# Performance work log

Hardware: AMD Instinct MI355X
Metric: run time of the kernel (lower is better)

Reference implementation:

```python
import jax, jax.numpy as jnp
import numpy as np

B, D, NH = 32768, 32, 128
SCALE = 0.05  # weight init scale; keeps exp(s) well-conditioned


def setup_inputs() -> dict:
    key = jax.random.key(0)
    ks = jax.random.split(key, 10)
    x = jax.random.normal(ks[0], (B, D), jnp.float32)
    # layer 0: LeafParam(2) -> learned constant (s, t)
    p0 = jax.random.normal(ks[1], (2,), jnp.float32) * SCALE
    # per-dim MLPs for i = 1..D-1, stacked. Layer i consumes x[:, :i]; we pad
    # its first weight to (D, NH) with rows >= i zeroed so a single batched
    # einsum computes all per-dim nets at once (same math as the python loop).
    mask = (jnp.arange(D)[None, :] < jnp.arange(1, D)[:, None]).astype(jnp.float32)  # (D-1, D)
    W1 = jax.random.normal(ks[2], (D - 1, D, NH), jnp.float32) * SCALE * mask[:, :, None]
    b1 = jax.random.normal(ks[3], (D - 1, NH), jnp.float32) * SCALE
    W2 = jax.random.normal(ks[4], (D - 1, NH, NH), jnp.float32) * SCALE
    b2 = jax.random.normal(ks[5], (D - 1, NH), jnp.float32) * SCALE
    W3 = jax.random.normal(ks[6], (D - 1, NH, NH), jnp.float32) * SCALE
    b3 = jax.random.normal(ks[7], (D - 1, NH), jnp.float32) * SCALE
    W4 = jax.random.normal(ks[8], (D - 1, NH, 2), jnp.float32) * SCALE
    b4 = jax.random.normal(ks[9], (D - 1, 2), jnp.float32) * SCALE
    return dict(x=x, p0=p0, W1=W1, b1=b1, W2=W2, b2=b2, W3=W3, b3=b3, W4=W4, b4=b4)


def _lrelu(h):
    return jnp.where(h >= 0, h, 0.2 * h)  # LeakyReLU(0.2)


def reference(x, p0, W1, b1, W2, b2, W3, b3, W4, b4):
    # All D-1 per-dim MLPs in parallel. W1 rows >= i are zero, so
    h = _lrelu(jnp.einsum('bd,idh->bih', x, W1) + b1[None])     # (B, D-1, NH)
    h = _lrelu(jnp.einsum('bih,ihk->bik', h, W2) + b2[None])
    h = _lrelu(jnp.einsum('bih,ihk->bik', h, W3) + b3[None])
    st = jnp.einsum('bih,iho->bio', h, W4) + b4[None]           # (B, D-1, 2)
    st0 = jnp.broadcast_to(p0[None, None, :], (x.shape[0], 1, 2))
    st = jnp.concatenate([st0, st], axis=1)                     # (B, D, 2)
    s, t = st[..., 0], st[..., 1]
    z = x * jnp.exp(s) + t      # parity=True -> order is the identity permutation
    log_det = jnp.sum(s, axis=1)                                # (B,)
    return z, log_det
```

## Files before the change

### kernel.cpp

```cpp
#include <hip/hip_runtime.h>

typedef __bf16 v8bf  __attribute__((ext_vector_type(8)));
typedef float  f32x4  __attribute__((ext_vector_type(4)));
typedef float  f32x16 __attribute__((ext_vector_type(16)));
typedef unsigned int u32;
typedef u32 u32x4 __attribute__((ext_vector_type(4)));
typedef unsigned short u16;

#define NI   31
#define DD   32
#define NHID 128
#define NROW 32768
#define NCHUNK 32
#define ITERS  4
#define NET_EL 36864
#define W2F_EL 4096
#define W3F_EL 20480
#define LDS_W4T 73728
#define LDS_BB  74240
#define LDS_BYTES 75008

__device__ __forceinline__ u32 cvtpk(float lo, float hi) {
    u32 r;
    asm("v_cvt_pk_bf16_f32 %0, %1, %2" : "=v"(r) : "v"(lo), "v"(hi));
    return r;
}

__device__ __forceinline__ void repack_tile(const f32x16 c, v8bf* f0, v8bf* f1) {
    f32x16 v;
    #pragma unroll
    for (int r = 0; r < 16; ++r) { float x = c[r]; v[r] = fmaxf(x, 0.2f * x); }
    #pragma unroll
    for (int p = 0; p < 2; ++p) {
        u32 a0 = cvtpk(v[8*p + 0], v[8*p + 1]);
        u32 a1 = cvtpk(v[8*p + 2], v[8*p + 3]);
        u32 b0 = cvtpk(v[8*p + 4], v[8*p + 5]);
        u32 b1 = cvtpk(v[8*p + 6], v[8*p + 7]);
        asm("v_permlane32_swap_b32 %0, %1" : "+v"(a0), "+v"(b0));
        asm("v_permlane32_swap_b32 %0, %1" : "+v"(a1), "+v"(b1));
        u32x4 wd = {a0, a1, b0, b1};
        if (p == 0) *f0 = __builtin_bit_cast(v8bf, wd);
        else        *f1 = __builtin_bit_cast(v8bf, wd);
    }
}

__global__ void maf_prep(const float* __restrict__ W1, const float* __restrict__ W2,
                         const float* __restrict__ W3, __bf16* __restrict__ blob,
                         __bf16* __restrict__ xfrag, float* __restrict__ xT,
                         const float* __restrict__ x, const float* __restrict__ p0,
                         float* __restrict__ zout, float* __restrict__ ldout) {
    int b = blockIdx.x, t = threadIdx.x;
    if (b < 3 * NI) {
        __shared__ float panel[16 * 128];
        int kind = b / NI, i = b % NI;
        const float* src; __bf16* dst; int NKS;
        if (kind == 0)      { src = W2 + (size_t)i * NHID * NHID; dst = blob + (size_t)i * NET_EL + W2F_EL; NKS = 8; }
        else if (kind == 1) { src = W3 + (size_t)i * NHID * NHID; dst = blob + (size_t)i * NET_EL + W3F_EL; NKS = 8; }
        else                { src = W1 + (size_t)i * DD * NHID;   dst = blob + (size_t)i * NET_EL;          NKS = 2; }
        const int fo = t & 127, hi2 = t >> 7;
        const int mt = fo >> 5, c = fo & 31;
        for (int ksb = 0; ksb < NKS; ++ksb) {
            #pragma unroll
            for (int r = 0; r < 8; ++r) {
                int e = r * 256 + t;
                panel[e] = src[(size_t)(ksb * 16 + (e >> 7)) * NHID + (e & 127)];
            }
            __syncthreads();
            __bf16 tmp[8];
            #pragma unroll
            for (int j = 0; j < 8; ++j) tmp[j] = (__bf16)panel[(hi2 * 8 + j) * 128 + fo];
            *(u32x4*)&dst[((size_t)(mt * NKS + ksb) * 64 + hi2 * 32 + c) * 8] = *(u32x4*)tmp;
            __syncthreads();
        }
    } else {
        __shared__ float pan[64 * 33];
        const int xb = b - 3 * NI;
        const float s0 = p0[0], t0 = p0[1];
        const float es = expf(s0);
        for (int pass = 0; pass < 4; ++pass) {
            const int rb = xb * 256 + pass * 64;
            #pragma unroll
            for (int r = 0; r < 8; ++r) {
                int e = r * 256 + t;
                pan[(e >> 5) * 33 + (e & 31)] = x[(size_t)(rb + (e >> 5)) * DD + (e & 31)];
            }
            __syncthreads();
            {
                int row = t & 63, dbase = (t >> 6) * 8;
                #pragma unroll
                for (int dd = 0; dd < 8; ++dd)
                    xT[(size_t)(dbase + dd) * NROW + rb + row] = pan[row * 33 + dbase + dd];
            }
            {
                int w2 = t >> 6, l = t & 63;
                int nt = w2 >> 1, ks = w2 & 1;
                int c = l & 31, hi = l >> 5;
                const float* pr = &pan[(nt * 32 + c) * 33 + ks * 16 + hi * 8];
                f32x4 x0 = *(const f32x4*)pr;
                f32x4 x1 = *(const f32x4*)(pr + 4);
                u32x4 wd = {cvtpk(x0[0], x0[1]), cvtpk(x0[2], x0[3]),
                            cvtpk(x1[0], x1[1]), cvtpk(x1[2], x1[3])};
                *(u32x4*)&xfrag[(size_t)(rb >> 6) * 2048 + ((w2 * 64 + l) << 3)] = wd;
            }
            if (t < 64) {
                int row = rb + t;
                ldout[row] = s0;
                zout[(size_t)row * DD] = pan[t * 33] * es + t0;
            }
            __syncthreads();
        }
    }
}

__global__ __launch_bounds__(256, 2) void maf_main(
    const __bf16* __restrict__ xfrag, const float* __restrict__ xT,
    const __bf16* __restrict__ blob,
    const float* __restrict__ b1, const float* __restrict__ b2,
    const float* __restrict__ b3,
    const float* __restrict__ W4, const float* __restrict__ b4,
    float* __restrict__ zout, float* __restrict__ ldout) {

    extern __shared__ __align__(16) char smem[];
    __bf16* w4t = (__bf16*)(smem + LDS_W4T);
    __bf16* bb  = (__bf16*)(smem + LDS_BB);
    const __bf16* wlds = (const __bf16*)smem;

    const int t = threadIdx.x;
    const int i = blockIdx.x / NCHUNK;
    const int chunk = blockIdx.x % NCHUNK;
    const int l = t & 63, w = t >> 6, c = l & 31, hi = l >> 5;
    const bool full_k1 = (i >= 16);

    {
        const u32x4* src = (const u32x4*)(blob + (size_t)i * NET_EL);
        u32x4* dst = (u32x4*)smem;
        #pragma unroll
        for (int k = 0; k < 18; ++k) dst[k * 256 + t] = src[k * 256 + t];
        w4t[t] = (__bf16)W4[(size_t)i * 2 * NHID + (t & 127) * 2 + (t >> 7)];
        if (t < NHID) {
            bb[t]       = (__bf16)b1[i * NHID + t];
            bb[128 + t] = (__bf16)b2[i * NHID + t];
            bb[256 + t] = (__bf16)b3[i * NHID + t];
        }
    }
    __syncthreads();

    const u32 ones0 = (hi == 0) ? 0x3F80u : 0u;
    const v8bf Bones = __builtin_bit_cast(v8bf, (u32x4){ones0, 0u, 0u, 0u});
    const float s0 = b4[2 * i], t0 = b4[2 * i + 1];
    const f32x16 zz = {};

    f32x16 acc[4][2];
    v8bf Bf[2][8];
    v8bf Bx[2][2];

#define LOADX(G)                                                                      \
    { const __bf16* xg = xfrag + (size_t)(G) * 2048;                                  \
      Bx[0][0] = *(const v8bf*)&xg[(0 * 64 + l) << 3];                                \
      if (full_k1) Bx[0][1] = *(const v8bf*)&xg[(1 * 64 + l) << 3];                   \
      Bx[1][0] = *(const v8bf*)&xg[(2 * 64 + l) << 3];                                \
      if (full_k1) Bx[1][1] = *(const v8bf*)&xg[(3 * 64 + l) << 3]; }

#define ABIAS(BOFF, MT)                                                               \
    __builtin_bit_cast(v8bf, (u32x4){                                                 \
        (hi == 0) ? (u32)__builtin_bit_cast(u16, bb[(BOFF) + (MT) * 32 + c]) : 0u,    \
        0u, 0u, 0u})

#define HIDDEN(BASE_EL, BOFF)                                                         \
    {                                                                                 \
        _Pragma("unroll")                                                             \
        for (int mt = 0; mt < 4; ++mt) {                                              \
            v8bf Ab = ABIAS(BOFF, mt);                                                \
            acc[mt][0] = __builtin_amdgcn_mfma_f32_32x32x16_bf16(Ab, Bones, zz, 0, 0, 0); \
            acc[mt][1] = __builtin_amdgcn_mfma_f32_32x32x16_bf16(Ab, Bones, zz, 0, 0, 0); \
        }                                                                             \
        _Pragma("unroll")                                                             \
        for (int ks = 0; ks < 8; ++ks) {                                              \
            v8bf A[4];                                                                \
            _Pragma("unroll")                                                         \
            for (int mt = 0; mt < 4; ++mt)                                            \
                A[mt] = *(const v8bf*)&wlds[(BASE_EL) + ((mt * 8 + ks) * 64 + l) * 8]; \
            _Pragma("unroll")                                                         \
            for (int mt = 0; mt < 4; ++mt)                                            \
                _Pragma("unroll")                                                     \
                for (int nt = 0; nt < 2; ++nt)                                        \
                    acc[mt][nt] = __builtin_amdgcn_mfma_f32_32x32x16_bf16(            \
                        A[mt], Bf[nt][ks], acc[mt][nt], 0, 0, 0);                     \
        }                                                                             \
        _Pragma("unroll")                                                             \
        for (int mt = 0; mt < 4; ++mt)                                                \
            _Pragma("unroll")                                                         \
            for (int nt = 0; nt < 2; ++nt)                                            \
                repack_tile(acc[mt][nt], &Bf[nt][2 * mt], &Bf[nt][2 * mt + 1]);       \
    }

    LOADX((chunk * 1024 + w * 64) >> 6)

    for (int it = 0; it < ITERS; ++it) {
        const int row0 = chunk * 1024 + it * 256 + w * 64;

        #pragma unroll
        for (int mt = 0; mt < 4; ++mt) {
            v8bf Ab = ABIAS(0, mt);
            v8bf A0 = *(const v8bf*)&wlds[((mt * 2 + 0) * 64 + l) * 8];
            v8bf A1;
            if (full_k1) A1 = *(const v8bf*)&wlds[((mt * 2 + 1) * 64 + l) * 8];
            #pragma unroll
            for (int nt = 0; nt < 2; ++nt) {
                f32x16 a = __builtin_amdgcn_mfma_f32_32x32x16_bf16(Ab, Bones, zz, 0, 0, 0);
                a = __builtin_amdgcn_mfma_f32_32x32x16_bf16(A0, Bx[nt][0], a, 0, 0, 0);
                if (full_k1)
                    a = __builtin_amdgcn_mfma_f32_32x32x16_bf16(A1, Bx[nt][1], a, 0, 0, 0);
                acc[mt][nt] = a;
            }
        }
        #pragma unroll
        for (int mt = 0; mt < 4; ++mt)
            #pragma unroll
            for (int nt = 0; nt < 2; ++nt)
                repack_tile(acc[mt][nt], &Bf[nt][2 * mt], &Bf[nt][2 * mt + 1]);

        if (it + 1 < ITERS)
            LOADX((chunk * 1024 + (it + 1) * 256 + w * 64) >> 6)

        HIDDEN(W2F_EL, 128)
        HIDDEN(W3F_EL, 256)

        {
            f32x16 acc4[2];
            acc4[0] = zz; acc4[1] = zz;
            #pragma unroll
            for (int ks = 0; ks < 8; ++ks) {
                v8bf a4 = {};
                if (c < 2) a4 = *(const v8bf*)&w4t[c * NHID + ks * 16 + hi * 8];
                acc4[0] = __builtin_amdgcn_mfma_f32_32x32x16_bf16(a4, Bf[0][ks], acc4[0], 0, 0, 0);
                acc4[1] = __builtin_amdgcn_mfma_f32_32x32x16_bf16(a4, Bf[1][ks], acc4[1], 0, 0, 0);
            }
            if (hi == 0) {
                #pragma unroll
                for (int nt = 0; nt < 2; ++nt) {
                    int row = row0 + nt * 32 + c;
                    float s  = acc4[nt][0] + s0;
                    float tt = acc4[nt][1] + t0;
                    float xv = xT[(size_t)(i + 1) * NROW + row];
                    zout[(size_t)row * DD + i + 1] = xv * expf(s) + tt;
                    atomicAdd(&ldout[row], s);
                }
            }
        }
    }
#undef LOADX
#undef ABIAS
#undef HIDDEN
}

extern "C" void kernel_launch(void* const* d_in, const int* in_sizes, int n_in,
                              void* d_out, int out_size, void* d_ws, size_t ws_size,
                              hipStream_t stream) {
    (void)in_sizes; (void)n_in; (void)out_size; (void)ws_size;
    const float* x  = (const float*)d_in[0];
    const float* p0 = (const float*)d_in[1];
    const float* W1 = (const float*)d_in[2];
    const float* b1 = (const float*)d_in[3];
    const float* W2 = (const float*)d_in[4];
    const float* b2 = (const float*)d_in[5];
    const float* W3 = (const float*)d_in[6];
    const float* b3 = (const float*)d_in[7];
    const float* W4 = (const float*)d_in[8];
    const float* b4 = (const float*)d_in[9];

    float* zout  = (float*)d_out;
    float* ldout = zout + (size_t)NROW * DD;

    __bf16* blob  = (__bf16*)d_ws;
    __bf16* xfrag = blob + (size_t)NI * NET_EL;
    float*  xT    = (float*)(xfrag + (size_t)NROW * DD);

    hipFuncSetAttribute((const void*)maf_main,
                        hipFuncAttributeMaxDynamicSharedMemorySize, LDS_BYTES);

    maf_prep<<<3 * NI + 128, 256, 0, stream>>>(W1, W2, W3, blob, xfrag, xT,
                                               x, p0, zout, ldout);
    maf_main<<<NI * NCHUNK, 256, LDS_BYTES, stream>>>(xfrag, xT, blob,
                                                      b1, b2, b3, W4, b4, zout, ldout);
}
```

Before: 98.69 us.

## Split epilogue into finalize kernel, shrink LDS, read W1/W3 from global

The main kernel no longer writes z with strided stores or does atomicAdd for log_det. It now stores per-net s (fp32) and t (bf16) into transposed scratch buffers, and a new finalize kernel reduces log_det and writes z coalesced through LDS. Only W2 is staged in LDS; W1 and W3 fragments are read directly from global/L2, which cuts LDS use. That could allow more blocks per CU, and the grid is doubled with half the iterations per block. The trade-offs are an extra kernel launch, an extra scratch round-trip, bf16 rounding of t, and global-latency weight loads in the inner loops.

```diff
diff --git a/kernel.cpp b/kernel.cpp
--- a/kernel.cpp
+++ b/kernel.cpp
@@ -11,14 +11,11 @@
 #define DD   32
 #define NHID 128
 #define NROW 32768
-#define NCHUNK 32
-#define ITERS  4
+#define NCHUNK 64
+#define ITERS  2
 #define NET_EL 36864
 #define W2F_EL 4096
 #define W3F_EL 20480
-#define LDS_W4T 73728
-#define LDS_BB  74240
-#define LDS_BYTES 75008
 
 __device__ __forceinline__ u32 cvtpk(float lo, float hi) {
     u32 r;
@@ -46,9 +43,7 @@
 
 __global__ void maf_prep(const float* __restrict__ W1, const float* __restrict__ W2,
                          const float* __restrict__ W3, __bf16* __restrict__ blob,
-                         __bf16* __restrict__ xfrag, float* __restrict__ xT,
-                         const float* __restrict__ x, const float* __restrict__ p0,
-                         float* __restrict__ zout, float* __restrict__ ldout) {
+                         __bf16* __restrict__ xfrag, const float* __restrict__ x) {
     int b = blockIdx.x, t = threadIdx.x;
     if (b < 3 * NI) {
         __shared__ float panel[16 * 128];
@@ -75,8 +70,6 @@
     } else {
         __shared__ float pan[64 * 33];
         const int xb = b - 3 * NI;
-        const float s0 = p0[0], t0 = p0[1];
-        const float es = expf(s0);
         for (int pass = 0; pass < 4; ++pass) {
             const int rb = xb * 256 + pass * 64;
             #pragma unroll
@@ -85,12 +78,6 @@
                 pan[(e >> 5) * 33 + (e & 31)] = x[(size_t)(rb + (e >> 5)) * DD + (e & 31)];
             }
             __syncthreads();
-            {
-                int row = t & 63, dbase = (t >> 6) * 8;
-                #pragma unroll
-                for (int dd = 0; dd < 8; ++dd)
-                    xT[(size_t)(dbase + dd) * NROW + rb + row] = pan[row * 33 + dbase + dd];
-            }
             {
                 int w2 = t >> 6, l = t & 63;
                 int nt = w2 >> 1, ks = w2 & 1;
@@ -102,28 +89,21 @@
                             cvtpk(x1[0], x1[1]), cvtpk(x1[2], x1[3])};
                 *(u32x4*)&xfrag[(size_t)(rb >> 6) * 2048 + ((w2 * 64 + l) << 3)] = wd;
             }
-            if (t < 64) {
-                int row = rb + t;
-                ldout[row] = s0;
-                zout[(size_t)row * DD] = pan[t * 33] * es + t0;
-            }
             __syncthreads();
         }
     }
 }
 
 __global__ __launch_bounds__(256, 2) void maf_main(
-    const __bf16* __restrict__ xfrag, const float* __restrict__ xT,
-    const __bf16* __restrict__ blob,
+    const __bf16* __restrict__ xfrag, const __bf16* __restrict__ blob,
     const float* __restrict__ b1, const float* __restrict__ b2,
     const float* __restrict__ b3,
     const float* __restrict__ W4, const float* __restrict__ b4,
-    float* __restrict__ zout, float* __restrict__ ldout) {
-
-    extern __shared__ __align__(16) char smem[];
-    __bf16* w4t = (__bf16*)(smem + LDS_W4T);
-    __bf16* bb  = (__bf16*)(smem + LDS_BB);
-    const __bf16* wlds = (const __bf16*)smem;
+    float* __restrict__ sT, __bf16* __restrict__ tT) {
+
+    __shared__ __align__(16) __bf16 w2s[16384];
+    __shared__ __align__(16) __bf16 w4t[2 * NHID];
+    __shared__ __align__(16) __bf16 bb[3 * NHID];
 
     const int t = threadIdx.x;
     const int i = blockIdx.x / NCHUNK;
@@ -131,24 +111,8 @@
     const int l = t & 63, w = t >> 6, c = l & 31, hi = l >> 5;
     const bool full_k1 = (i >= 16);
 
-    {
-        const u32x4* src = (const u32x4*)(blob + (size_t)i * NET_EL);
-        u32x4* dst = (u32x4*)smem;
-        #pragma unroll
-        for (int k = 0; k < 18; ++k) dst[k * 256 + t] = src[k * 256 + t];
-        w4t[t] = (__bf16)W4[(size_t)i * 2 * NHID + (t & 127) * 2 + (t >> 7)];
-        if (t < NHID) {
-            bb[t]       = (__bf16)b1[i * NHID + t];
-            bb[128 + t] = (__bf16)b2[i * NHID + t];
-            bb[256 + t] = (__bf16)b3[i * NHID + t];
-        }
-    }
-    __syncthreads();
-
-    const u32 ones0 = (hi == 0) ? 0x3F80u : 0u;
-    const v8bf Bones = __builtin_bit_cast(v8bf, (u32x4){ones0, 0u, 0u, 0u});
-    const float s0 = b4[2 * i], t0 = b4[2 * i + 1];
-    const f32x16 zz = {};
+    const __bf16* wg1 = blob + (size_t)i * NET_EL;
+    const __bf16* wg3 = blob + (size_t)i * NET_EL + W3F_EL;
 
     f32x16 acc[4][2];
     v8bf Bf[2][8];
@@ -161,12 +125,33 @@
       Bx[1][0] = *(const v8bf*)&xg[(2 * 64 + l) << 3];                                \
       if (full_k1) Bx[1][1] = *(const v8bf*)&xg[(3 * 64 + l) << 3]; }
 
+    LOADX((chunk * (ITERS * 256) + w * 64) >> 6)
+
+    {
+        const u32x4* src = (const u32x4*)(blob + (size_t)i * NET_EL + W2F_EL);
+        u32x4* dst = (u32x4*)w2s;
+        #pragma unroll
+        for (int k = 0; k < 8; ++k) dst[k * 256 + t] = src[k * 256 + t];
+        w4t[t] = (__bf16)W4[(size_t)i * 2 * NHID + (t & 127) * 2 + (t >> 7)];
+        if (t < NHID) {
+            bb[t]       = (__bf16)b1[i * NHID + t];
+            bb[128 + t] = (__bf16)b2[i * NHID + t];
+            bb[256 + t] = (__bf16)b3[i * NHID + t];
+        }
+    }
+    __syncthreads();
+
+    const u32 ones0 = (hi == 0) ? 0x3F80u : 0u;
+    const v8bf Bones = __builtin_bit_cast(v8bf, (u32x4){ones0, 0u, 0u, 0u});
+    const float s0 = b4[2 * i], t0 = b4[2 * i + 1];
+    const f32x16 zz = {};
+
 #define ABIAS(BOFF, MT)                                                               \
     __builtin_bit_cast(v8bf, (u32x4){                                                 \
         (hi == 0) ? (u32)__builtin_bit_cast(u16, bb[(BOFF) + (MT) * 32 + c]) : 0u,    \
         0u, 0u, 0u})
 
-#define HIDDEN(BASE_EL, BOFF)                                                         \
+#define HIDDEN(WP, BOFF)                                                              \
     {                                                                                 \
         _Pragma("unroll")                                                             \
         for (int mt = 0; mt < 4; ++mt) {                                              \
@@ -179,7 +164,7 @@
             v8bf A[4];                                                                \
             _Pragma("unroll")                                                         \
             for (int mt = 0; mt < 4; ++mt)                                            \
-                A[mt] = *(const v8bf*)&wlds[(BASE_EL) + ((mt * 8 + ks) * 64 + l) * 8]; \
+                A[mt] = *(const v8bf*)&(WP)[((mt * 8 + ks) * 64 + l) * 8];            \
             _Pragma("unroll")                                                         \
             for (int mt = 0; mt < 4; ++mt)                                            \
                 _Pragma("unroll")                                                     \
@@ -194,17 +179,15 @@
                 repack_tile(acc[mt][nt], &Bf[nt][2 * mt], &Bf[nt][2 * mt + 1]);       \
     }
 
-    LOADX((chunk * 1024 + w * 64) >> 6)
-
     for (int it = 0; it < ITERS; ++it) {
-        const int row0 = chunk * 1024 + it * 256 + w * 64;
+        const int row0 = chunk * (ITERS * 256) + it * 256 + w * 64;
 
         #pragma unroll
         for (int mt = 0; mt < 4; ++mt) {
             v8bf Ab = ABIAS(0, mt);
-            v8bf A0 = *(const v8bf*)&wlds[((mt * 2 + 0) * 64 + l) * 8];
+            v8bf A0 = *(const v8bf*)&wg1[((mt * 2 + 0) * 64 + l) * 8];
             v8bf A1;
-            if (full_k1) A1 = *(const v8bf*)&wlds[((mt * 2 + 1) * 64 + l) * 8];
+            if (full_k1) A1 = *(const v8bf*)&wg1[((mt * 2 + 1) * 64 + l) * 8];
             #pragma unroll
             for (int nt = 0; nt < 2; ++nt) {
                 f32x16 a = __builtin_amdgcn_mfma_f32_32x32x16_bf16(Ab, Bones, zz, 0, 0, 0);
@@ -221,10 +204,10 @@
                 repack_tile(acc[mt][nt], &Bf[nt][2 * mt], &Bf[nt][2 * mt + 1]);
 
         if (it + 1 < ITERS)
-            LOADX((chunk * 1024 + (it + 1) * 256 + w * 64) >> 6)
-
-        HIDDEN(W2F_EL, 128)
-        HIDDEN(W3F_EL, 256)
+            LOADX((chunk * (ITERS * 256) + (it + 1) * 256 + w * 64) >> 6)
+
+        HIDDEN(w2s, 128)
+        HIDDEN(wg3, 256)
 
         {
             f32x16 acc4[2];
@@ -240,11 +223,8 @@
                 #pragma unroll
                 for (int nt = 0; nt < 2; ++nt) {
                     int row = row0 + nt * 32 + c;
-                    float s  = acc4[nt][0] + s0;
-                    float tt = acc4[nt][1] + t0;
-                    float xv = xT[(size_t)(i + 1) * NROW + row];
-                    zout[(size_t)row * DD + i + 1] = xv * expf(s) + tt;
-                    atomicAdd(&ldout[row], s);
+                    sT[(size_t)i * NROW + row] = acc4[nt][0] + s0;
+                    tT[(size_t)i * NROW + row] = (__bf16)(acc4[nt][1] + t0);
                 }
             }
         }
@@ -252,6 +232,38 @@
 #undef LOADX
 #undef ABIAS
 #undef HIDDEN
+}
+
+__global__ void maf_fin(const float* __restrict__ x, const float* __restrict__ p0,
+                        const float* __restrict__ sT, const __bf16* __restrict__ tT,
+                        float* __restrict__ zout, float* __restrict__ ldout) {
+    __shared__ float zsm[4 * 64 * 33];
+    const int t = threadIdx.x, w = t >> 6, l = t & 63;
+    const int rowbase = blockIdx.x * 256 + w * 64;
+    const int row = rowbase + l;
+    float* zs = zsm + w * (64 * 33);
+
+    float xr[DD];
+    #pragma unroll
+    for (int q = 0; q < 8; ++q)
+        *(f32x4*)&xr[q * 4] = *(const f32x4*)&x[(size_t)row * DD + q * 4];
+
+    const float s0 = p0[0], t0 = p0[1];
+    float ld = s0;
+    zs[l * 33] = xr[0] * expf(s0) + t0;
+    #pragma unroll
+    for (int i = 0; i < NI; ++i) {
+        float s  = sT[(size_t)i * NROW + row];
+        float tt = (float)tT[(size_t)i * NROW + row];
+        ld += s;
+        zs[l * 33 + i + 1] = xr[i + 1] * expf(s) + tt;
+    }
+    ldout[row] = ld;
+    #pragma unroll
+    for (int j = 0; j < 32; ++j) {
+        int f = j * 64 + l;
+        zout[(size_t)rowbase * DD + f] = zs[(f >> 5) * 33 + (f & 31)];
+    }
 }
 
 extern "C" void kernel_launch(void* const* d_in, const int* in_sizes, int n_in,
@@ -274,13 +286,10 @@
 
     __bf16* blob  = (__bf16*)d_ws;
     __bf16* xfrag = blob + (size_t)NI * NET_EL;
-    float*  xT    = (float*)(xfrag + (size_t)NROW * DD);
-
-    hipFuncSetAttribute((const void*)maf_main,
-                        hipFuncAttributeMaxDynamicSharedMemorySize, LDS_BYTES);
-
-    maf_prep<<<3 * NI + 128, 256, 0, stream>>>(W1, W2, W3, blob, xfrag, xT,
-                                               x, p0, zout, ldout);
-    maf_main<<<NI * NCHUNK, 256, LDS_BYTES, stream>>>(xfrag, xT, blob,
-                                                      b1, b2, b3, W4, b4, zout, ldout);
-}
+    float*  sT    = (float*)(xfrag + (size_t)NROW * DD);
+    __bf16* tT    = (__bf16*)(sT + (size_t)NI * NROW);
+
+    maf_prep<<<3 * NI + 128, 256, 0, stream>>>(W1, W2, W3, blob, xfrag, x);
+    maf_main<<<NI * NCHUNK, 256, 0, stream>>>(xfrag, blob, b1, b2, b3, W4, b4, sT, tT);
+    maf_fin<<<NROW / 256, 256, 0, stream>>>(x, p0, sT, tT, zout, ldout);
+}
```

Measured after the change: 152.0 us. 54.0% more time.
